# Kernel tuning notes

Measured on AMD Instinct MI355X. Metric: run time of the kernel, lower is better.

## Reference

```python
import jax, jax.numpy as jnp
import numpy as np

N_NODES = 50000
N_EDGES = 800000
D_IN = 64
D_OUT = 64


def setup_inputs() -> dict:
    key = jax.random.key(0)
    ks = jax.random.split(key, 7)
    features = jax.random.normal(ks[0], (N_NODES, D_IN), dtype=jnp.float32)
    # Linear(in,out,bias=False) weight: (out_features, in_features)
    W = jax.random.normal(ks[1], (D_OUT, D_IN), dtype=jnp.float32) / np.sqrt(D_IN)
    bias = jnp.zeros((D_OUT,), dtype=jnp.float32)
    skip_weight = jnp.ones((D_OUT,), dtype=jnp.float32)
    # sparse normalized adjacency as an edge list with scalar weights
    edge_src = jax.random.randint(ks[2], (N_EDGES,), 0, N_NODES, dtype=jnp.int32)
    edge_dst = jax.random.randint(ks[3], (N_EDGES,), 0, N_NODES, dtype=jnp.int32)
    edge_weight = jax.random.uniform(ks[4], (N_EDGES,), dtype=jnp.float32)
    return {
        "features": features,
        "W": W,
        "bias": bias,
        "skip_weight": skip_weight,
        "edge_weight": edge_weight,
        "edge_src": edge_src,
        "edge_dst": edge_dst,
    }


def reference(features, W, bias, skip_weight, edge_weight, edge_src, edge_dst):
    # Feature transform: x @ W^T  -> (n, out_features)
    h = jnp.einsum("nd,od->no", features, W)
    # Skip term: elementwise scale of transformed features
    skip = h * skip_weight
    # Sparse SpMM: aggregate weighted neighbor messages
    msgs = h[edge_src] * edge_weight[:, None]          # (E, out)
    agg = jax.ops.segment_sum(msgs, edge_dst, num_segments=N_NODES)  # (n, out)
    out = skip + agg + bias
    return jax.nn.selu(out)
```

## Files before the change

kernel.cpp:

```cpp
#include <hip/hip_runtime.h>
#include <math.h>

#define N_NODES 50000
#define N_EDGES 800000
#define D 64
#define NB2 782
#define BCAP2 2048
#define EPB 4096
#define NSCAT 196
#define CAPB 32
#define SLAB (NSCAT * CAPB)
#define GROWS 128
#define NGEMM ((N_NODES + GROWS - 1) / GROWS)

__device__ __forceinline__ float selu_f(float x) {
    const float scale = 1.0507009873554805f;
    const float alpha = 1.6732632423543772f;
    return x > 0.0f ? scale * x : scale * alpha * expm1f(x);
}

__device__ __forceinline__ unsigned int f2bf(float x) {
    unsigned int u = __float_as_uint(x);
    u += 0x7FFFu + ((u >> 16) & 1u);
    return u >> 16;
}

__device__ __forceinline__ float bf2f(unsigned int b) {
    return __uint_as_float(b << 16);
}

__global__ __launch_bounds__(1024) void fused_gemm_scatter(const float* __restrict__ feat,
                                                           const float* __restrict__ W,
                                                           const int* __restrict__ edst,
                                                           const int* __restrict__ esrc,
                                                           const float* __restrict__ ew,
                                                           unsigned short* __restrict__ hb,
                                                           int* __restrict__ cnts,
                                                           int2* __restrict__ pay) {
    extern __shared__ char smem[];
    const int tid = threadIdx.x;

    if (blockIdx.x < NSCAT) {
        int* hist    = (int*)smem;
        int* lexcl   = hist + NB2;
        int* waveAgg = lexcl + NB2;
        int2* stage  = (int2*)(waveAgg + 16);

        const int wid = tid >> 6;
        const int lane = tid & 63;
        const int e0 = blockIdx.x * EPB;
        const int cntb = min(EPB, N_EDGES - e0);

        for (int i = tid; i < NB2; i += 1024) hist[i] = 0;
        __syncthreads();

        int2 rec[4];
        int rb[4];
#pragma unroll
        for (int k = 0; k < 4; ++k) {
            const int idx = k * 1024 + tid;
            rb[k] = -1;
            if (idx < cntb) {
                const int e = e0 + idx;
                const int dst = edst[e];
                const int b = dst >> 6;
                rb[k] = b;
                rec[k] = make_int2((esrc[e] & 0xFFFF) | ((dst & 63) << 16) | (b << 22),
                                   __float_as_int(ew[e]));
                atomicAdd(&hist[b], 1);
            }
        }
        __syncthreads();

        const int v = (tid < NB2) ? hist[tid] : 0;
        int incl = v;
#pragma unroll
        for (int off = 1; off < 64; off <<= 1) {
            const int t = __shfl_up(incl, off);
            if (lane >= off) incl += t;
        }
        if (lane == 63) waveAgg[wid] = incl;
        __syncthreads();
        if (wid == 0) {
            const int wv = (lane < 16) ? waveAgg[lane] : 0;
            int wincl = wv;
#pragma unroll
            for (int off = 1; off < 16; off <<= 1) {
                const int t = __shfl_up(wincl, off);
                if (lane >= off) wincl += t;
            }
            if (lane < 16) waveAgg[lane] = wincl - wv;
        }
        __syncthreads();
        if (tid < NB2) {
            const int excl = incl - v + waveAgg[wid];
            lexcl[tid] = excl;
            hist[tid] = excl;
            cnts[blockIdx.x * NB2 + tid] = v;
        }
        __syncthreads();

#pragma unroll
        for (int k = 0; k < 4; ++k) {
            if (rb[k] >= 0) {
                const int p = atomicAdd(&hist[rb[k]], 1);
                stage[p] = rec[k];
            }
        }
        __syncthreads();

        for (int i = tid; i < cntb; i += 1024) {
            const int2 r = stage[i];
            const int b = ((unsigned int)r.x) >> 22;
            const int off = i - lexcl[b];
            if (off < CAPB) pay[(size_t)b * SLAB + blockIdx.x * CAPB + off] = r;
        }
    } else {
        float* Wt = (float*)smem;
        float* Sf = Wt + 64 * 68;
        const int base = (blockIdx.x - NSCAT) * GROWS;

        for (int i = tid; i < D * D; i += 1024) {
            int o = i >> 6, d = i & 63;
            Wt[d * 68 + o] = W[i];
        }
        for (int i = tid; i < GROWS * D; i += 1024) {
            int r = i >> 6, c = i & 63;
            int row = base + r;
            Sf[r * 68 + c] = (row < N_NODES) ? feat[(size_t)row * D + c] : 0.0f;
        }
        __syncthreads();

        const int r = tid >> 3;
        const int cg = tid & 7;
        const int row = base + r;
        if (row >= N_NODES) return;

        float4 a0 = {0, 0, 0, 0}, a1 = {0, 0, 0, 0};
        const float* WtC = Wt + cg * 8;
        const float* SfR = Sf + r * 68;
#pragma unroll 8
        for (int k = 0; k < D; ++k) {
            const float f = SfR[k];
            const float4 w0 = *(const float4*)(WtC + k * 68);
            const float4 w1 = *(const float4*)(WtC + k * 68 + 4);
            a0.x += f * w0.x; a0.y += f * w0.y; a0.z += f * w0.z; a0.w += f * w0.w;
            a1.x += f * w1.x; a1.y += f * w1.y; a1.z += f * w1.z; a1.w += f * w1.w;
        }

        uint4 p;
        p.x = f2bf(a0.x) | (f2bf(a0.y) << 16);
        p.y = f2bf(a0.z) | (f2bf(a0.w) << 16);
        p.z = f2bf(a1.x) | (f2bf(a1.y) << 16);
        p.w = f2bf(a1.z) | (f2bf(a1.w) << 16);
        *(uint4*)(hb + (size_t)row * D + cg * 8) = p;
    }
}

__global__ __launch_bounds__(512) void csr_sort(const int* __restrict__ cnts,
                                                int2* __restrict__ pay,
                                                int2* __restrict__ nodeinfo) {
    __shared__ int2 stage[BCAP2];
    __shared__ int cntS[NSCAT];
    __shared__ int runoff[NSCAT];
    __shared__ int waveAgg[8];
    __shared__ int cntL[64], curL[64];

    const int b = blockIdx.x;
    const int tid = threadIdx.x;
    const int wid = tid >> 6;
    const int lane = tid & 63;
    int2* payb = pay + (size_t)b * SLAB;

    if (tid < 64) cntL[tid] = 0;

    const int c = (tid < NSCAT) ? cnts[tid * NB2 + b] : 0;

    int incl = c;
#pragma unroll
    for (int off = 1; off < 64; off <<= 1) {
        const int t = __shfl_up(incl, off);
        if (lane >= off) incl += t;
    }
    if (lane == 63) waveAgg[wid] = incl;
    __syncthreads();
    if (wid == 0) {
        const int wv = (lane < 8) ? waveAgg[lane] : 0;
        int wincl = wv;
#pragma unroll
        for (int off = 1; off < 8; off <<= 1) {
            const int t = __shfl_up(wincl, off);
            if (lane >= off) wincl += t;
        }
        if (lane < 8) waveAgg[lane] = wincl - wv;
    }
    __syncthreads();
    if (tid < NSCAT) {
        cntS[tid] = c;
        runoff[tid] = incl - c + waveAgg[wid];
    }
    __syncthreads();

    for (int i = tid; i < NSCAT * CAPB; i += 512) {
        const int blk = i >> 5;
        const int pos = i & (CAPB - 1);
        if (pos < cntS[blk]) {
            const int p = runoff[blk] + pos;
            if (p < BCAP2) {
                const int2 r = payb[i];
                stage[p] = r;
                atomicAdd(&cntL[(r.x >> 16) & 63], 1);
            }
        }
    }
    __syncthreads();

    const int total = min(runoff[NSCAT - 1] + cntS[NSCAT - 1], BCAP2);

    if (tid < 64) {
        const int v = cntL[tid];
        int inc2 = v;
#pragma unroll
        for (int off = 1; off < 64; off <<= 1) {
            const int t = __shfl_up(inc2, off);
            if (tid >= off) inc2 += t;
        }
        const int excl = inc2 - v;
        curL[tid] = excl;
        const int node = (b << 6) + tid;
        if (node < N_NODES) nodeinfo[node] = make_int2(b * SLAB + excl, v);
    }
    __syncthreads();

    for (int i = tid; i < total; i += 512) {
        const int2 r = stage[i];
        const int p = atomicAdd(&curL[(r.x >> 16) & 63], 1);
        payb[p] = r;
    }
}

__global__ __launch_bounds__(256) void agg_epilogue_kernel(const unsigned short* __restrict__ hb,
                                                           const int2* __restrict__ nodeinfo,
                                                           const int2* __restrict__ pay,
                                                           const float* __restrict__ bias,
                                                           const float* __restrict__ skipw,
                                                           float* __restrict__ out) {
    const int gtid = blockIdx.x * 256 + threadIdx.x;
    const int n = gtid >> 6;
    const int lane = gtid & 63;
    if (n >= N_NODES) return;

    const int half = lane >> 5;
    const int sl = lane & 31;

    const int2 info = nodeinfo[n];
    const int beg = info.x;
    const int deg = info.y;

    float a0x = 0.f, a0y = 0.f, a1x = 0.f, a1y = 0.f;
    float a2x = 0.f, a2y = 0.f, a3x = 0.f, a3y = 0.f;

    for (int i = 0; i < deg; i += 64) {
        const int cnt = min(64, deg - i);
        int2 sw = make_int2(0, 0);
        if (lane < cnt) sw = pay[beg + i + lane];

        int j = 0;
        for (; j + 7 < cnt; j += 8) {
            const int s0 = __shfl(sw.x, j + 0 + half) & 0xFFFF;
            const int s1 = __shfl(sw.x, j + 2 + half) & 0xFFFF;
            const int s2 = __shfl(sw.x, j + 4 + half) & 0xFFFF;
            const int s3 = __shfl(sw.x, j + 6 + half) & 0xFFFF;
            const float w0 = __int_as_float(__shfl(sw.y, j + 0 + half));
            const float w1 = __int_as_float(__shfl(sw.y, j + 2 + half));
            const float w2 = __int_as_float(__shfl(sw.y, j + 4 + half));
            const float w3 = __int_as_float(__shfl(sw.y, j + 6 + half));
            const unsigned int g0 = *(const unsigned int*)(hb + ((size_t)s0 << 6) + sl * 2);
            const unsigned int g1 = *(const unsigned int*)(hb + ((size_t)s1 << 6) + sl * 2);
            const unsigned int g2 = *(const unsigned int*)(hb + ((size_t)s2 << 6) + sl * 2);
            const unsigned int g3 = *(const unsigned int*)(hb + ((size_t)s3 << 6) + sl * 2);
            a0x += bf2f(g0 & 0xFFFF) * w0;  a0y += bf2f(g0 >> 16) * w0;
            a1x += bf2f(g1 & 0xFFFF) * w1;  a1y += bf2f(g1 >> 16) * w1;
            a2x += bf2f(g2 & 0xFFFF) * w2;  a2y += bf2f(g2 >> 16) * w2;
            a3x += bf2f(g3 & 0xFFFF) * w3;  a3y += bf2f(g3 >> 16) * w3;
        }
        for (; j + 1 < cnt; j += 2) {
            const int s = __shfl(sw.x, j + half) & 0xFFFF;
            const float w = __int_as_float(__shfl(sw.y, j + half));
            const unsigned int g = *(const unsigned int*)(hb + ((size_t)s << 6) + sl * 2);
            a0x += bf2f(g & 0xFFFF) * w;  a0y += bf2f(g >> 16) * w;
        }
        if (j < cnt) {
            const int s = __shfl(sw.x, j) & 0xFFFF;
            const float w = __int_as_float(__shfl(sw.y, j));
            const unsigned int g = *(const unsigned int*)(hb + ((size_t)s << 6) + sl * 2);
            const float m = (half == 0) ? 1.0f : 0.0f;
            a1x += bf2f(g & 0xFFFF) * w * m;  a1y += bf2f(g >> 16) * w * m;
        }
    }

    float sx = (a0x + a1x) + (a2x + a3x);
    float sy = (a0y + a1y) + (a2y + a3y);
    sx += __shfl_xor(sx, 32);
    sy += __shfl_xor(sy, 32);

    const unsigned int hn = *(const unsigned int*)(hb + ((size_t)n << 6) + sl * 2);
    const float2 kv = ((const float2*)skipw)[sl];
    const float2 bv = ((const float2*)bias)[sl];
    if (half == 0) {
        float2 o;
        o.x = selu_f(bf2f(hn & 0xFFFF) * kv.x + bv.x + sx);
        o.y = selu_f(bf2f(hn >> 16) * kv.y + bv.y + sy);
        ((float2*)(out + ((size_t)n << 6)))[sl] = o;
    }
}

extern "C" void kernel_launch(void* const* d_in, const int* in_sizes, int n_in,
                              void* d_out, int out_size, void* d_ws, size_t ws_size,
                              hipStream_t stream) {
    const float* feat  = (const float*)d_in[0];
    const float* W     = (const float*)d_in[1];
    const float* bias  = (const float*)d_in[2];
    const float* skipw = (const float*)d_in[3];
    const float* ew    = (const float*)d_in[4];
    const int*   esrc  = (const int*)d_in[5];
    const int*   edst  = (const int*)d_in[6];
    float* out = (float*)d_out;

    int2*           pay      = (int2*)d_ws;
    unsigned short* hb       = (unsigned short*)(pay + (size_t)NB2 * SLAB);
    int2*           nodeinfo = (int2*)(hb + (size_t)N_NODES * D);
    int*            cnts     = (int*)(nodeinfo + N_NODES);

    const size_t smem = (size_t)(64 * 68 + GROWS * 68) * sizeof(float);
    fused_gemm_scatter<<<NSCAT + NGEMM, 1024, smem, stream>>>(feat, W, edst, esrc, ew,
                                                              hb, cnts, pay);

    csr_sort<<<NB2, 512, 0, stream>>>(cnts, pay, nodeinfo);

    agg_epilogue_kernel<<<(N_NODES * 64 + 255) / 256, 256, 0, stream>>>(
        hb, nodeinfo, pay, bias, skipw, out);
}
```

Before: 131.4 us.

## Fuse CSR bucket sort with aggregation epilogue, keeping sorted edges in LDS

Merges the per-bucket sort kernel and the aggregation/SELU epilogue into one kernel. Each 1024-thread block sorts its 64-node bucket's edges into shared memory, and each wave then aggregates 4 nodes directly from LDS. This removes the write-back of sorted payload, the nodeinfo array, one kernel launch and the re-read of the payload from global memory. In exchange, the aggregation phase runs on only 782 blocks with 16 waves each and higher LDS use per block, which lowers the parallelism available to hide gather latency.

```diff
diff --git a/kernel.cpp b/kernel.cpp
--- a/kernel.cpp
+++ b/kernel.cpp
@@ -157,22 +157,26 @@
     }
 }
 
-__global__ __launch_bounds__(512) void csr_sort(const int* __restrict__ cnts,
-                                                int2* __restrict__ pay,
-                                                int2* __restrict__ nodeinfo) {
+__global__ __launch_bounds__(1024) void sort_agg(const int* __restrict__ cnts,
+                                                 const int2* __restrict__ pay,
+                                                 const unsigned short* __restrict__ hb,
+                                                 const float* __restrict__ bias,
+                                                 const float* __restrict__ skipw,
+                                                 float* __restrict__ out) {
     __shared__ int2 stage[BCAP2];
+    __shared__ int2 sorted[BCAP2];
     __shared__ int cntS[NSCAT];
     __shared__ int runoff[NSCAT];
-    __shared__ int waveAgg[8];
-    __shared__ int cntL[64], curL[64];
+    __shared__ int waveAgg[16];
+    __shared__ int cntB[64], begB[64], curB[64];
 
     const int b = blockIdx.x;
     const int tid = threadIdx.x;
     const int wid = tid >> 6;
     const int lane = tid & 63;
-    int2* payb = pay + (size_t)b * SLAB;
-
-    if (tid < 64) cntL[tid] = 0;
+    const int2* payb = pay + (size_t)b * SLAB;
+
+    if (tid < 64) cntB[tid] = 0;
 
     const int c = (tid < NSCAT) ? cnts[tid * NB2 + b] : 0;
 
@@ -185,14 +189,14 @@
     if (lane == 63) waveAgg[wid] = incl;
     __syncthreads();
     if (wid == 0) {
-        const int wv = (lane < 8) ? waveAgg[lane] : 0;
+        const int wv = (lane < 16) ? waveAgg[lane] : 0;
         int wincl = wv;
 #pragma unroll
-        for (int off = 1; off < 8; off <<= 1) {
+        for (int off = 1; off < 16; off <<= 1) {
             const int t = __shfl_up(wincl, off);
             if (lane >= off) wincl += t;
         }
-        if (lane < 8) waveAgg[lane] = wincl - wv;
+        if (lane < 16) waveAgg[lane] = wincl - wv;
     }
     __syncthreads();
     if (tid < NSCAT) {
@@ -201,7 +205,7 @@
     }
     __syncthreads();
 
-    for (int i = tid; i < NSCAT * CAPB; i += 512) {
+    for (int i = tid; i < NSCAT * CAPB; i += 1024) {
         const int blk = i >> 5;
         const int pos = i & (CAPB - 1);
         if (pos < cntS[blk]) {
@@ -209,7 +213,7 @@
             if (p < BCAP2) {
                 const int2 r = payb[i];
                 stage[p] = r;
-                atomicAdd(&cntL[(r.x >> 16) & 63], 1);
+                atomicAdd(&cntB[(r.x >> 16) & 63], 1);
             }
         }
     }
@@ -218,7 +222,7 @@
     const int total = min(runoff[NSCAT - 1] + cntS[NSCAT - 1], BCAP2);
 
     if (tid < 64) {
-        const int v = cntL[tid];
+        const int v = cntB[tid];
         int inc2 = v;
 #pragma unroll
         for (int off = 1; off < 64; off <<= 1) {
@@ -226,92 +230,79 @@
             if (tid >= off) inc2 += t;
         }
         const int excl = inc2 - v;
-        curL[tid] = excl;
-        const int node = (b << 6) + tid;
-        if (node < N_NODES) nodeinfo[node] = make_int2(b * SLAB + excl, v);
-    }
-    __syncthreads();
-
-    for (int i = tid; i < total; i += 512) {
+        begB[tid] = excl;
+        curB[tid] = excl;
+    }
+    __syncthreads();
+
+    for (int i = tid; i < total; i += 1024) {
         const int2 r = stage[i];
-        const int p = atomicAdd(&curL[(r.x >> 16) & 63], 1);
-        payb[p] = r;
-    }
-}
-
-__global__ __launch_bounds__(256) void agg_epilogue_kernel(const unsigned short* __restrict__ hb,
-                                                           const int2* __restrict__ nodeinfo,
-                                                           const int2* __restrict__ pay,
-                                                           const float* __restrict__ bias,
-                                                           const float* __restrict__ skipw,
-                                                           float* __restrict__ out) {
-    const int gtid = blockIdx.x * 256 + threadIdx.x;
-    const int n = gtid >> 6;
-    const int lane = gtid & 63;
-    if (n >= N_NODES) return;
+        const int p = atomicAdd(&curB[(r.x >> 16) & 63], 1);
+        sorted[p] = r;
+    }
+    __syncthreads();
 
     const int half = lane >> 5;
     const int sl = lane & 31;
-
-    const int2 info = nodeinfo[n];
-    const int beg = info.x;
-    const int deg = info.y;
-
-    float a0x = 0.f, a0y = 0.f, a1x = 0.f, a1y = 0.f;
-    float a2x = 0.f, a2y = 0.f, a3x = 0.f, a3y = 0.f;
-
-    for (int i = 0; i < deg; i += 64) {
-        const int cnt = min(64, deg - i);
-        int2 sw = make_int2(0, 0);
-        if (lane < cnt) sw = pay[beg + i + lane];
+    const float2 kv = ((const float2*)skipw)[sl];
+    const float2 bv = ((const float2*)bias)[sl];
+
+    for (int nn = 0; nn < 4; ++nn) {
+        const int nl = wid * 4 + nn;
+        const int node = (b << 6) + nl;
+        if (node >= N_NODES) break;
+
+        const int beg = begB[nl];
+        const int deg = cntB[nl];
+
+        float a0x = 0.f, a0y = 0.f, a1x = 0.f, a1y = 0.f;
+        float a2x = 0.f, a2y = 0.f, a3x = 0.f, a3y = 0.f;
 
         int j = 0;
-        for (; j + 7 < cnt; j += 8) {
-            const int s0 = __shfl(sw.x, j + 0 + half) & 0xFFFF;
-            const int s1 = __shfl(sw.x, j + 2 + half) & 0xFFFF;
-            const int s2 = __shfl(sw.x, j + 4 + half) & 0xFFFF;
-            const int s3 = __shfl(sw.x, j + 6 + half) & 0xFFFF;
-            const float w0 = __int_as_float(__shfl(sw.y, j + 0 + half));
-            const float w1 = __int_as_float(__shfl(sw.y, j + 2 + half));
-            const float w2 = __int_as_float(__shfl(sw.y, j + 4 + half));
-            const float w3 = __int_as_float(__shfl(sw.y, j + 6 + half));
-            const unsigned int g0 = *(const unsigned int*)(hb + ((size_t)s0 << 6) + sl * 2);
-            const unsigned int g1 = *(const unsigned int*)(hb + ((size_t)s1 << 6) + sl * 2);
-            const unsigned int g2 = *(const unsigned int*)(hb + ((size_t)s2 << 6) + sl * 2);
-            const unsigned int g3 = *(const unsigned int*)(hb + ((size_t)s3 << 6) + sl * 2);
+        for (; j + 7 < deg; j += 8) {
+            const int2 r0 = sorted[beg + j + 0 + half];
+            const int2 r1 = sorted[beg + j + 2 + half];
+            const int2 r2 = sorted[beg + j + 4 + half];
+            const int2 r3 = sorted[beg + j + 6 + half];
+            const unsigned int g0 = *(const unsigned int*)(hb + ((size_t)(r0.x & 0xFFFF) << 6) + sl * 2);
+            const unsigned int g1 = *(const unsigned int*)(hb + ((size_t)(r1.x & 0xFFFF) << 6) + sl * 2);
+            const unsigned int g2 = *(const unsigned int*)(hb + ((size_t)(r2.x & 0xFFFF) << 6) + sl * 2);
+            const unsigned int g3 = *(const unsigned int*)(hb + ((size_t)(r3.x & 0xFFFF) << 6) + sl * 2);
+            const float w0 = __int_as_float(r0.y);
+            const float w1 = __int_as_float(r1.y);
+            const float w2 = __int_as_float(r2.y);
+            const float w3 = __int_as_float(r3.y);
             a0x += bf2f(g0 & 0xFFFF) * w0;  a0y += bf2f(g0 >> 16) * w0;
             a1x += bf2f(g1 & 0xFFFF) * w1;  a1y += bf2f(g1 >> 16) * w1;
             a2x += bf2f(g2 & 0xFFFF) * w2;  a2y += bf2f(g2 >> 16) * w2;
             a3x += bf2f(g3 & 0xFFFF) * w3;  a3y += bf2f(g3 >> 16) * w3;
         }
-        for (; j + 1 < cnt; j += 2) {
-            const int s = __shfl(sw.x, j + half) & 0xFFFF;
-            const float w = __int_as_float(__shfl(sw.y, j + half));
-            const unsigned int g = *(const unsigned int*)(hb + ((size_t)s << 6) + sl * 2);
+        for (; j + 1 < deg; j += 2) {
+            const int2 r = sorted[beg + j + half];
+            const unsigned int g = *(const unsigned int*)(hb + ((size_t)(r.x & 0xFFFF) << 6) + sl * 2);
+            const float w = __int_as_float(r.y);
             a0x += bf2f(g & 0xFFFF) * w;  a0y += bf2f(g >> 16) * w;
         }
-        if (j < cnt) {
-            const int s = __shfl(sw.x, j) & 0xFFFF;
-            const float w = __int_as_float(__shfl(sw.y, j));
-            const unsigned int g = *(const unsigned int*)(hb + ((size_t)s << 6) + sl * 2);
+        if (j < deg) {
+            const int2 r = sorted[beg + j];
+            const unsigned int g = *(const unsigned int*)(hb + ((size_t)(r.x & 0xFFFF) << 6) + sl * 2);
+            const float w = __int_as_float(r.y);
             const float m = (half == 0) ? 1.0f : 0.0f;
             a1x += bf2f(g & 0xFFFF) * w * m;  a1y += bf2f(g >> 16) * w * m;
         }
-    }
-
-    float sx = (a0x + a1x) + (a2x + a3x);
-    float sy = (a0y + a1y) + (a2y + a3y);
-    sx += __shfl_xor(sx, 32);
-    sy += __shfl_xor(sy, 32);
-
-    const unsigned int hn = *(const unsigned int*)(hb + ((size_t)n << 6) + sl * 2);
-    const float2 kv = ((const float2*)skipw)[sl];
-    const float2 bv = ((const float2*)bias)[sl];
-    if (half == 0) {
-        float2 o;
-        o.x = selu_f(bf2f(hn & 0xFFFF) * kv.x + bv.x + sx);
-        o.y = selu_f(bf2f(hn >> 16) * kv.y + bv.y + sy);
-        ((float2*)(out + ((size_t)n << 6)))[sl] = o;
+
+        float sx = (a0x + a1x) + (a2x + a3x);
+        float sy = (a0y + a1y) + (a2y + a3y);
+        sx += __shfl_xor(sx, 32);
+        sy += __shfl_xor(sy, 32);
+
+        if (half == 0) {
+            const unsigned int hn = *(const unsigned int*)(hb + ((size_t)node << 6) + sl * 2);
+            float2 o;
+            o.x = selu_f(bf2f(hn & 0xFFFF) * kv.x + bv.x + sx);
+            o.y = selu_f(bf2f(hn >> 16) * kv.y + bv.y + sy);
+            ((float2*)(out + ((size_t)node << 6)))[sl] = o;
+        }
     }
 }
 
@@ -327,17 +318,13 @@
     const int*   edst  = (const int*)d_in[6];
     float* out = (float*)d_out;
 
-    int2*           pay      = (int2*)d_ws;
-    unsigned short* hb       = (unsigned short*)(pay + (size_t)NB2 * SLAB);
-    int2*           nodeinfo = (int2*)(hb + (size_t)N_NODES * D);
-    int*            cnts     = (int*)(nodeinfo + N_NODES);
+    int2*           pay  = (int2*)d_ws;
+    unsigned short* hb   = (unsigned short*)(pay + (size_t)NB2 * SLAB);
+    int*            cnts = (int*)(hb + (size_t)N_NODES * D);
 
     const size_t smem = (size_t)(64 * 68 + GROWS * 68) * sizeof(float);
     fused_gemm_scatter<<<NSCAT + NGEMM, 1024, smem, stream>>>(feat, W, edst, esrc, ew,
                                                               hb, cnts, pay);
 
-    csr_sort<<<NB2, 512, 0, stream>>>(cnts, pay, nodeinfo);
-
-    agg_epilogue_kernel<<<(N_NODES * 64 + 255) / 256, 256, 0, stream>>>(
-        hb, nodeinfo, pay, bias, skipw, out);
-}
+    sort_agg<<<NB2, 1024, 0, stream>>>(cnts, pay, hb, bias, skipw, out);
+}
```

New measurement: 126.2 us. -4.0%, faster.
